# Optimization experiments

Measured on AMD Instinct MI355X. Metric: run time of the kernel, lower is better.

Reference implementation:

```python
import jax, jax.numpy as jnp
import numpy as np

B, N, T, D = 4, 256, 64, 128
DR, DH = 32, 128  # d_relation, d_hidden


def setup_inputs() -> dict:
    key = jax.random.key(0)
    ks = jax.random.split(key, 12)
    s = 0.05
    return {
        "H": jax.random.normal(ks[0], (B, N, T, D), jnp.float32),
        "R": jax.random.normal(ks[1], (B, N, N, DR), jnp.float32),
        "delta_H": jax.random.normal(ks[2], (B, N, T, D), jnp.float32),
        # params (torch Linear convention: W @ x + b with W shape (out, in))
        "Wq": jax.random.normal(ks[3], (DH, D), jnp.float32) * s,
        "bq": jnp.zeros((DH,), jnp.float32),
        "Wk": jax.random.normal(ks[4], (DH, D), jnp.float32) * s,
        "bk": jnp.zeros((DH,), jnp.float32),
        "Wr": jax.random.normal(ks[5], (DH, DR), jnp.float32) * s,
        "br": jnp.zeros((DH,), jnp.float32),
        "Wf": jax.random.normal(ks[6], (D, 3 * D + DR), jnp.float32) * s,
        "bf": jnp.zeros((D,), jnp.float32),
        "gamma": jnp.ones((D,), jnp.float32),
        "beta": jnp.zeros((D,), jnp.float32),
    }


def reference(H, R, delta_H, Wq, bq, Wk, bk, Wr, br, Wf, bf, gamma, beta):
    Bm, Nn, Tt, Dd = H.shape
    dr = R.shape[-1]

    # projections (eval mode: dropout is identity)
    q = jnp.einsum('bitd,hd->bith', H, Wq) + bq           # (B,N,T,DH)
    k = jnp.einsum('bjtd,hd->bjth', H, Wk) + bk           # (B,N,T,DH)
    rproj = jnp.einsum('bijr,hr->bijh', R, Wr) + br       # (B,N,N,DH)

    # attn_score[b,i,j,t] = <q_i[t], k_j[t] + Wr(r_ij)> / sqrt(d_model)
    scores = (jnp.einsum('bith,bjth->bijt', q, k)
              + jnp.einsum('bith,bijh->bijt', q, rproj)) / jnp.sqrt(jnp.asarray(Dd, H.dtype))
    w = jax.nn.softmax(scores, axis=-1)                   # softmax over time t
    # exclude the j == i pair (original loop skips it)
    w = w * (1.0 - jnp.eye(Nn, dtype=w.dtype))[None, :, :, None]

    # fuse Linear decomposed over the concat [h_i, h_j, r_ij, sum_t delta_h_j]
    W1 = Wf[:, :Dd]                 # acts on h_i
    W2 = Wf[:, Dd:2 * Dd]           # acts on h_j
    W3 = Wf[:, 2 * Dd:2 * Dd + dr]  # acts on r_ij
    W4 = Wf[:, 2 * Dd + dr:]        # acts on delta sum

    A = jnp.einsum('bitd,ed->bite', H, W1)                       # (B,N,T,D)
    Bj = jnp.einsum('bjtd,ed->bjte', H, W2)                      # (B,N,T,D)
    Cij = jnp.einsum('bijr,er->bije', R, W3)                     # (B,N,N,D)
    Ej = jnp.einsum('bjd,ed->bje', delta_H.sum(axis=2), W4)      # (B,N,D)

    wsum = w.sum(axis=2)                                         # (B,N,T)
    z = ((A + bf) * wsum[..., None]
         + jnp.einsum('bijt,bjte->bite', w, Bj)
         + jnp.einsum('bijt,bije->bite', w, Cij)
         + jnp.einsum('bijt,bje->bite', w, Ej))

    # residual + LayerNorm over last dim
    x = H + z
    mu = x.mean(axis=-1, keepdims=True)
    var = x.var(axis=-1, keepdims=True)
    return (x - mu) / jnp.sqrt(var + 1e-5) * gamma + beta
```

## Files before the change

### kernel.cpp

```cpp
#include <hip/hip_runtime.h>

typedef __attribute__((ext_vector_type(4))) float f32x4;
typedef __attribute__((ext_vector_type(8))) short short8;

constexpr int NB = 4, NS = 256, NT = 64, ND = 128, NR = 32;
constexpr int WFR = 3 * ND + NR;
constexpr float SCALE = 0.08838834764831845f;

__device__ __forceinline__ unsigned short f2bf(float f) {
  unsigned x = __float_as_uint(f);
  return (unsigned short)((x + 0x7FFFu + ((x >> 16) & 1u)) >> 16);
}
__device__ __forceinline__ float bf2f(unsigned short u) {
  return __uint_as_float((unsigned)u << 16);
}

__global__ __launch_bounds__(256) void kP(const float* __restrict__ Wq,
    const float* __restrict__ Wk, const float* __restrict__ Wr,
    const float* __restrict__ br, const float* __restrict__ bq,
    const float* __restrict__ Wf,
    unsigned short* __restrict__ Wqb, unsigned short* __restrict__ Wkb,
    unsigned short* __restrict__ W1b, unsigned short* __restrict__ W2b,
    unsigned short* __restrict__ W3b, unsigned short* __restrict__ Wqrt,
    float* __restrict__ Gbias) {
  const int blk = blockIdx.x, tid = threadIdx.x;
  if (blk < 64) {
    const int which = blk >> 4;
    const int idx = ((blk & 15) * 256 + tid) * 4;
    const int e = idx >> 7, d = idx & 127;
    float4 v;
    unsigned short* dst;
    if (which == 0)      { v = *(const float4*)&Wq[idx];            dst = Wqb; }
    else if (which == 1) { v = *(const float4*)&Wk[idx];            dst = Wkb; }
    else if (which == 2) { v = *(const float4*)&Wf[e * WFR + d];        dst = W1b; }
    else                 { v = *(const float4*)&Wf[e * WFR + ND + d];   dst = W2b; }
    dst[idx + 0] = f2bf(v.x); dst[idx + 1] = f2bf(v.y);
    dst[idx + 2] = f2bf(v.z); dst[idx + 3] = f2bf(v.w);
  } else if (blk < 68) {
    const int idx = ((blk - 64) * 256 + tid) * 4;
    const int e = idx >> 5, r = idx & 31;
    float4 v = *(const float4*)&Wf[e * WFR + 2 * ND + r];
    W3b[idx + 0] = f2bf(v.x); W3b[idx + 1] = f2bf(v.y);
    W3b[idx + 2] = f2bf(v.z); W3b[idx + 3] = f2bf(v.w);
  } else {
    const int rr = blk - 68;
    __shared__ float Vl[128];
    __shared__ float gbl[128];
    if (tid < 128) {
      float v = 0.f;
      if (rr < 32) v = Wr[tid * 32 + rr];
      else if (rr == 32) v = br[tid];
      Vl[tid] = v;
      gbl[tid] = bq[tid] * v;
    }
    __syncthreads();
    if (tid < 128) {
      float acc = 0.f;
      #pragma unroll 8
      for (int h = 0; h < 128; ++h) acc += Wq[h * 128 + tid] * Vl[h];
      Wqrt[rr * 128 + tid] = f2bf(acc * SCALE);
    }
    if (tid == 0) {
      float g = 0.f;
      for (int h = 0; h < 128; ++h) g += gbl[h];
      Gbias[rr] = g * SCALE;
    }
  }
}

__global__ __launch_bounds__(128) void kA(const float* __restrict__ dH,
                                          const float* __restrict__ Wf,
                                          float* __restrict__ Ej) {
  __shared__ float ds[ND];
  const int bj = blockIdx.x;
  const int d = threadIdx.x;
  const float* p = dH + (size_t)bj * NT * ND + d;
  float s = 0.f;
  #pragma unroll 8
  for (int t = 0; t < NT; ++t) s += p[t * ND];
  ds[d] = s;
  __syncthreads();
  const float* w4 = Wf + (size_t)d * WFR + 2 * ND + NR;
  float acc = 0.f;
  #pragma unroll 8
  for (int dd = 0; dd < ND; ++dd) acc += ds[dd] * w4[dd];
  Ej[(size_t)bj * ND + d] = acc;
}

__global__ __launch_bounds__(256) void kR(const float* __restrict__ R,
                                          unsigned short* __restrict__ Rb,
                                          unsigned short* __restrict__ Rtb) {
  __shared__ unsigned short rt[256 * 34];
  const int bi = blockIdx.x, tid = threadIdx.x;
  const float* src = R + (size_t)bi * 8192;
  #pragma unroll
  for (int it = 0; it < 8; ++it) {
    const int idx = (tid + it * 256) * 4;
    const float4 v = *(const float4*)&src[idx];
    const unsigned short s0 = f2bf(v.x), s1 = f2bf(v.y);
    const unsigned short s2 = f2bf(v.z), s3 = f2bf(v.w);
    unsigned long long p = (unsigned long long)s0 | ((unsigned long long)s1 << 16)
                         | ((unsigned long long)s2 << 32) | ((unsigned long long)s3 << 48);
    *(unsigned long long*)&Rb[(size_t)bi * 8192 + idx] = p;
    const int j = idx >> 5, r = idx & 31;
    *(unsigned*)&rt[j * 34 + r]     = (unsigned)s0 | ((unsigned)s1 << 16);
    *(unsigned*)&rt[j * 34 + r + 2] = (unsigned)s2 | ((unsigned)s3 << 16);
  }
  __syncthreads();
  #pragma unroll
  for (int it = 0; it < 4; ++it) {
    const int flat = (tid + it * 256) * 8;
    const int r = flat >> 8, j0 = flat & 255;
    short8 o;
    #pragma unroll
    for (int u = 0; u < 8; ++u) o[u] = (short)rt[(j0 + u) * 34 + r];
    *(short8*)&Rtb[(size_t)bi * 8192 + flat] = o;
  }
}

__device__ __forceinline__ void gemm_tile(const short8 (&afr)[4][4],
    const unsigned short* __restrict__ Wp, int nt, int l15, int l4,
    f32x4 (&acc)[4]) {
  #pragma unroll
  for (int mt = 0; mt < 4; ++mt) acc[mt] = (f32x4){0.f, 0.f, 0.f, 0.f};
  #pragma unroll
  for (int kt = 0; kt < 4; ++kt) {
    short8 bfr = *(const short8*)(Wp + (16 * nt + l15) * 128 + 32 * kt + 8 * l4);
    #pragma unroll
    for (int mt = 0; mt < 4; ++mt)
      acc[mt] = __builtin_amdgcn_mfma_f32_16x16x32_bf16(afr[mt][kt], bfr, acc[mt], 0, 0, 0);
  }
}

__global__ __launch_bounds__(256) void kB(const float* __restrict__ H,
    const unsigned short* __restrict__ Wqb, const unsigned short* __restrict__ Wkb,
    const unsigned short* __restrict__ W1b, const unsigned short* __restrict__ W2b,
    const unsigned short* __restrict__ Wqrt, const float* __restrict__ Gbias,
    const float* __restrict__ bq, const float* __restrict__ bk,
    const float* __restrict__ bf, const float* __restrict__ Ej,
    unsigned short* __restrict__ qb, unsigned short* __restrict__ kb,
    unsigned short* __restrict__ Apbb, unsigned short* __restrict__ BEb,
    unsigned short* __restrict__ Gb) {
  __shared__ unsigned short st[4][64 * 136];
  const int bn = blockIdx.x, tid = threadIdx.x;
  const int b = bn >> 8, n = bn & 255;
  const int lane = tid & 63, wv = tid >> 6;
  const int l15 = lane & 15, l4 = lane >> 4;
  short8 afr[4][4];
  const float* hb = H + (size_t)bn * (NT * ND);
  #pragma unroll
  for (int mt = 0; mt < 4; ++mt)
    #pragma unroll
    for (int kt = 0; kt < 4; ++kt) {
      const float* p = hb + (16 * mt + l15) * ND + 32 * kt + 8 * l4;
      float4 u0 = *(const float4*)p;
      float4 u1 = *(const float4*)(p + 4);
      short8 f;
      f[0] = (short)f2bf(u0.x); f[1] = (short)f2bf(u0.y);
      f[2] = (short)f2bf(u0.z); f[3] = (short)f2bf(u0.w);
      f[4] = (short)f2bf(u1.x); f[5] = (short)f2bf(u1.y);
      f[6] = (short)f2bf(u1.z); f[7] = (short)f2bf(u1.w);
      afr[mt][kt] = f;
    }
  f32x4 acc[4];
  #pragma unroll 1
  for (int pass = 0; pass < 4; ++pass) {
    const unsigned short* W = (pass == 0) ? Wqb : (pass == 1) ? Wkb
                            : (pass == 2) ? W1b : W2b;
    unsigned short* buf = st[pass];
    #pragma unroll
    for (int n2 = 0; n2 < 2; ++n2) {
      const int nt = 2 * wv + n2, c = 16 * nt + l15;
      gemm_tile(afr, W, nt, l15, l4, acc);
      const float bias = (pass == 0) ? bq[c] : (pass == 1) ? bk[c]
                       : (pass == 2) ? bf[c] : Ej[(size_t)bn * 128 + c];
      #pragma unroll
      for (int mt = 0; mt < 4; ++mt)
        #pragma unroll
        for (int jr = 0; jr < 4; ++jr)
          buf[(16 * mt + 4 * l4 + jr) * 136 + c] = f2bf(acc[mt][jr] + bias);
    }
  }
  if (wv < 3) {
    const int nt = wv, c = 16 * nt + l15;
    gemm_tile(afr, Wqrt, nt, l15, l4, acc);
    const float bias = Gbias[c];
    #pragma unroll
    for (int mt = 0; mt < 4; ++mt)
      #pragma unroll
      for (int jr = 0; jr < 4; ++jr) {
        const int tr = 16 * mt + 4 * l4 + jr;
        Gb[(size_t)bn * 3072 + tr * 48 + c] = f2bf(acc[mt][jr] + bias);
      }
  }
  __syncthreads();
  const int row0 = tid >> 4, col = 8 * (tid & 15);
  #pragma unroll
  for (int it = 0; it < 4; ++it) {
    const int row = row0 + it * 16;
    *(short8*)&qb[((size_t)(b * 64 + row) * 256 + n) * 128 + col] =
        *(const short8*)&st[0][row * 136 + col];
    *(short8*)&kb[((size_t)(b * 64 + row) * 256 + n) * 128 + col] =
        *(const short8*)&st[1][row * 136 + col];
    *(short8*)&Apbb[(size_t)bn * 8192 + row * 128 + col] =
        *(const short8*)&st[2][row * 136 + col];
    *(short8*)&BEb[((size_t)(b * 64 + row) * 256 + n) * 128 + col] =
        *(const short8*)&st[3][row * 136 + col];
  }
}

__global__ __launch_bounds__(512) void kC1(const unsigned short* __restrict__ qb,
    const unsigned short* __restrict__ kb, unsigned short* __restrict__ Sb) {
  __shared__ unsigned short st[8][32 * 136];
  const int bt = blockIdx.x, jq = blockIdx.y;
  const int tid = threadIdx.x, lane = tid & 63, wv = tid >> 6;
  const int l15 = lane & 15, l4 = lane >> 4;
  const unsigned short* qslice = qb + (size_t)bt * (256 * 128);
  const unsigned short* kslice = kb + (size_t)bt * (256 * 128);
  f32x4 acc[2][8];
  #pragma unroll
  for (int mi = 0; mi < 2; ++mi)
    #pragma unroll
    for (int nt = 0; nt < 8; ++nt) acc[mi][nt] = (f32x4){0.f, 0.f, 0.f, 0.f};
  #pragma unroll
  for (int kt = 0; kt < 4; ++kt) {
    short8 a[2], bb[8];
    #pragma unroll
    for (int mi = 0; mi < 2; ++mi) {
      const int i = 32 * wv + 16 * mi + l15;
      a[mi] = *(const short8*)(qslice + i * 128 + 32 * kt + 8 * l4);
    }
    #pragma unroll
    for (int nt = 0; nt < 8; ++nt) {
      const int j = 128 * jq + 16 * nt + l15;
      bb[nt] = *(const short8*)(kslice + j * 128 + 32 * kt + 8 * l4);
    }
    #pragma unroll
    for (int mi = 0; mi < 2; ++mi)
      #pragma unroll
      for (int nt = 0; nt < 8; ++nt)
        acc[mi][nt] = __builtin_amdgcn_mfma_f32_16x16x32_bf16(a[mi], bb[nt], acc[mi][nt], 0, 0, 0);
  }
  unsigned short* buf = st[wv];
  #pragma unroll
  for (int mi = 0; mi < 2; ++mi)
    #pragma unroll
    for (int nt = 0; nt < 8; ++nt)
      #pragma unroll
      for (int jr = 0; jr < 4; ++jr)
        buf[(16 * mi + 4 * l4 + jr) * 136 + 16 * nt + l15] =
            f2bf(acc[mi][nt][jr] * SCALE);
  #pragma unroll
  for (int it = 0; it < 8; ++it) {
    const int flat = lane * 8 + it * 512;
    const int row = flat >> 7, col = flat & 127;
    const int i = 32 * wv + row;
    *(short8*)&Sb[((size_t)bt * 256 + i) * 256 + 128 * jq + col] =
        *(const short8*)&buf[row * 136 + col];
  }
}

__global__ __launch_bounds__(256) void kSM(
    const unsigned short* __restrict__ Gb, const unsigned short* __restrict__ Rb,
    const unsigned short* __restrict__ Rtb, const unsigned short* __restrict__ Sb,
    const unsigned short* __restrict__ W3b, unsigned short* __restrict__ Apbb,
    unsigned short* __restrict__ Wbw) {
  __shared__ unsigned short wl[64 * 264];
  __shared__ unsigned short Ml[4][16 * 40];
  __shared__ float wred[4][64];
  __shared__ float wsl[64];
  const int bi = blockIdx.x, b = bi >> 8, i = bi & 255;
  const int tid = threadIdx.x, lane = tid & 63, wv = tid >> 6;
  const int l15 = lane & 15, l4 = lane >> 4;
  const f32x4 zz = (f32x4){0.f, 0.f, 0.f, 0.f};

  #pragma unroll
  for (int it = 0; it < 8; ++it) {
    const int flat = tid * 8 + it * 2048;
    const int t = flat >> 8, col = flat & 255;
    *(short8*)&wl[t * 264 + col] =
        *(const short8*)&Sb[(((size_t)b * 64 + t) * 256 + i) * 256 + col];
  }

  short8 ga[4];
  #pragma unroll
  for (int mt = 0; mt < 4; ++mt)
    ga[mt] = *(const short8*)(Gb + ((size_t)bi * 64 + 16 * mt + l15) * 48 + 8 * l4);
  f32x4 acc[4][4];
  #pragma unroll
  for (int nt = 0; nt < 4; ++nt) {
    const int j = 64 * wv + 16 * nt + l15;
    short8 rb = *(const short8*)(Rb + ((size_t)bi * 256 + j) * 32 + 8 * l4);
    #pragma unroll
    for (int mt = 0; mt < 4; ++mt)
      acc[mt][nt] = __builtin_amdgcn_mfma_f32_16x16x32_bf16(ga[mt], rb, zz, 0, 0, 0);
  }
  float qbr[4][4];
  #pragma unroll
  for (int mt = 0; mt < 4; ++mt)
    #pragma unroll
    for (int jr = 0; jr < 4; ++jr)
      qbr[mt][jr] = bf2f(Gb[((size_t)bi * 64 + 16 * mt + 4 * l4 + jr) * 48 + 32]);

  __syncthreads();

  #pragma unroll
  for (int mt = 0; mt < 4; ++mt)
    #pragma unroll
    for (int nt = 0; nt < 4; ++nt)
      #pragma unroll
      for (int jr = 0; jr < 4; ++jr)
        acc[mt][nt][jr] += bf2f(wl[(16 * mt + 4 * l4 + jr) * 264 + 64 * wv + 16 * nt + l15])
                         + qbr[mt][jr];

  #pragma unroll
  for (int nt = 0; nt < 4; ++nt) {
    float mx = -1e30f;
    #pragma unroll
    for (int mt = 0; mt < 4; ++mt)
      #pragma unroll
      for (int jr = 0; jr < 4; ++jr) mx = fmaxf(mx, acc[mt][nt][jr]);
    mx = fmaxf(mx, __shfl_xor(mx, 16));
    mx = fmaxf(mx, __shfl_xor(mx, 32));
    float sm = 0.f;
    #pragma unroll
    for (int mt = 0; mt < 4; ++mt)
      #pragma unroll
      for (int jr = 0; jr < 4; ++jr) {
        const float e = __expf(acc[mt][nt][jr] - mx);
        acc[mt][nt][jr] = e;
        sm += e;
      }
    sm += __shfl_xor(sm, 16);
    sm += __shfl_xor(sm, 32);
    const int j = 64 * wv + 16 * nt + l15;
    const float inv = (j == i) ? 0.f : 1.f / sm;
    #pragma unroll
    for (int mt = 0; mt < 4; ++mt)
      #pragma unroll
      for (int jr = 0; jr < 4; ++jr) acc[mt][nt][jr] *= inv;
  }

  float part[4][4];
  #pragma unroll
  for (int mt = 0; mt < 4; ++mt)
    #pragma unroll
    for (int jr = 0; jr < 4; ++jr) {
      float s = 0.f;
      #pragma unroll
      for (int nt = 0; nt < 4; ++nt) s += acc[mt][nt][jr];
      part[mt][jr] = s;
    }
  #pragma unroll
  for (int m = 1; m < 16; m <<= 1)
    #pragma unroll
    for (int mt = 0; mt < 4; ++mt)
      #pragma unroll
      for (int jr = 0; jr < 4; ++jr) part[mt][jr] += __shfl_xor(part[mt][jr], m);
  if (l15 == 0) {
    #pragma unroll
    for (int mt = 0; mt < 4; ++mt)
      #pragma unroll
      for (int jr = 0; jr < 4; ++jr) wred[wv][16 * mt + 4 * l4 + jr] = part[mt][jr];
  }

  #pragma unroll
  for (int mt = 0; mt < 4; ++mt)
    #pragma unroll
    for (int nt = 0; nt < 4; ++nt)
      #pragma unroll
      for (int jr = 0; jr < 4; ++jr)
        wl[(16 * mt + 4 * l4 + jr) * 264 + 64 * wv + 16 * nt + l15] =
            f2bf(acc[mt][nt][jr]);

  __syncthreads();

  if (tid < 64) wsl[tid] = wred[0][tid] + wred[1][tid] + wred[2][tid] + wred[3][tid];

  #pragma unroll
  for (int it = 0; it < 8; ++it) {
    const int flat = tid * 8 + it * 2048;
    const int t = flat >> 8, j = flat & 255;
    *(short8*)&Wbw[(((size_t)(b * 64 + t)) * 256 + i) * 256 + j] =
        *(const short8*)&wl[t * 264 + j];
  }

  f32x4 mac[2];
  mac[0] = zz; mac[1] = zz;
  #pragma unroll
  for (int kt = 0; kt < 8; ++kt) {
    short8 a = *(const short8*)&wl[(16 * wv + l15) * 264 + 32 * kt + 8 * l4];
    #pragma unroll
    for (int nt = 0; nt < 2; ++nt) {
      short8 bb = *(const short8*)(Rtb + ((size_t)bi * 32 + 16 * nt + l15) * 256 + 32 * kt + 8 * l4);
      mac[nt] = __builtin_amdgcn_mfma_f32_16x16x32_bf16(a, bb, mac[nt], 0, 0, 0);
    }
  }
  #pragma unroll
  for (int nt = 0; nt < 2; ++nt)
    #pragma unroll
    for (int jr = 0; jr < 4; ++jr)
      Ml[wv][(4 * l4 + jr) * 40 + 16 * nt + l15] = f2bf(mac[nt][jr]);
  asm volatile("s_waitcnt lgkmcnt(0)" ::: "memory");
  short8 a2 = *(const short8*)&Ml[wv][l15 * 40 + 8 * l4];
  f32x4 tac[8];
  #pragma unroll
  for (int nt = 0; nt < 8; ++nt) {
    short8 w3 = *(const short8*)(W3b + (16 * nt + l15) * 32 + 8 * l4);
    tac[nt] = __builtin_amdgcn_mfma_f32_16x16x32_bf16(a2, w3, zz, 0, 0, 0);
  }
  __syncthreads();

  const size_t abase = (size_t)bi * 8192;
  #pragma unroll
  for (int it = 0; it < 4; ++it) {
    const int flat = tid * 8 + it * 2048;
    const int row = flat >> 7, col = flat & 127;
    *(short8*)&wl[row * 136 + col] = *(const short8*)&Apbb[abase + flat];
  }
  __syncthreads();
  #pragma unroll
  for (int jr = 0; jr < 4; ++jr) {
    const int t = 16 * wv + 4 * l4 + jr;
    const float ws = wsl[t];
    #pragma unroll
    for (int nt = 0; nt < 8; ++nt) {
      const int e = 16 * nt + l15;
      const int off = t * 136 + e;
      wl[off] = f2bf(bf2f(wl[off]) * ws + tac[nt][jr]);
    }
  }
  __syncthreads();
  #pragma unroll
  for (int it = 0; it < 4; ++it) {
    const int flat = tid * 8 + it * 2048;
    const int row = flat >> 7, col = flat & 127;
    *(short8*)&Apbb[abase + flat] = *(const short8*)&wl[row * 136 + col];
  }
}

__global__ __launch_bounds__(512) void kD(const unsigned short* __restrict__ Wb,
    const unsigned short* __restrict__ BEb, const unsigned short* __restrict__ zacc,
    const float* __restrict__ H, const float* __restrict__ gamma,
    const float* __restrict__ beta, float* __restrict__ out) {
  __shared__ unsigned short Bl[128 * 264];
  const int bt = blockIdx.x;
  const int b = bt >> 6, t = bt & 63;
  const int tid = threadIdx.x, lane = tid & 63, wv = tid >> 6;
  const int l15 = lane & 15, l4 = lane >> 4;
  {
    const int j = tid >> 1, eh = (tid & 1) * 64;
    const unsigned short* src = BEb + (size_t)bt * (256 * 128) + j * 128 + eh;
    #pragma unroll
    for (int eg = 0; eg < 8; ++eg) {
      short8 v = *(const short8*)(src + 8 * eg);
      #pragma unroll
      for (int u = 0; u < 8; ++u)
        Bl[(eh + 8 * eg + u) * 264 + j] = (unsigned short)v[u];
    }
  }
  __syncthreads();
  f32x4 acc[2][8];
  #pragma unroll
  for (int m2 = 0; m2 < 2; ++m2)
    #pragma unroll
    for (int nt = 0; nt < 8; ++nt) acc[m2][nt] = (f32x4){0.f, 0.f, 0.f, 0.f};
  #pragma unroll
  for (int kt = 0; kt < 8; ++kt) {
    short8 a[2];
    #pragma unroll
    for (int m2 = 0; m2 < 2; ++m2) {
      const int i = 32 * wv + 16 * m2 + l15;
      a[m2] = *(const short8*)(Wb + ((size_t)(b * 64 + t) * 256 + i) * 256 + 32 * kt + 8 * l4);
    }
    #pragma unroll
    for (int nt = 0; nt < 8; ++nt) {
      short8 bb = *(const short8*)(&Bl[(16 * nt + l15) * 264 + 32 * kt + 8 * l4]);
      #pragma unroll
      for (int m2 = 0; m2 < 2; ++m2)
        acc[m2][nt] = __builtin_amdgcn_mfma_f32_16x16x32_bf16(a[m2], bb, acc[m2][nt], 0, 0, 0);
    }
  }
  float gam[8], bet[8];
  #pragma unroll
  for (int nt = 0; nt < 8; ++nt) {
    const int e = 16 * nt + l15;
    gam[nt] = gamma[e];
    bet[nt] = beta[e];
  }
  #pragma unroll
  for (int m2 = 0; m2 < 2; ++m2)
    #pragma unroll
    for (int jr = 0; jr < 4; ++jr) {
      const int i = 32 * wv + 16 * m2 + 4 * l4 + jr;
      const size_t base = ((size_t)(b * 256 + i) * 64 + t) * 128;
      float x[8];
      float sm = 0.f, sq = 0.f;
      #pragma unroll
      for (int nt = 0; nt < 8; ++nt) {
        const int e = 16 * nt + l15;
        const float v = acc[m2][nt][jr] + bf2f(zacc[base + e]) + H[base + e];
        x[nt] = v;
        sm += v;
        sq += v * v;
      }
      #pragma unroll
      for (int m = 1; m < 16; m <<= 1) {
        sm += __shfl_xor(sm, m);
        sq += __shfl_xor(sq, m);
      }
      const float mu = sm * (1.f / 128.f);
      const float inv = rsqrtf(sq * (1.f / 128.f) - mu * mu + 1e-5f);
      #pragma unroll
      for (int nt = 0; nt < 8; ++nt)
        out[base + 16 * nt + l15] = (x[nt] - mu) * inv * gam[nt] + bet[nt];
    }
}

extern "C" void kernel_launch(void* const* d_in, const int* in_sizes, int n_in,
                              void* d_out, int out_size, void* d_ws, size_t ws_size,
                              hipStream_t stream) {
  (void)in_sizes; (void)n_in; (void)out_size; (void)ws_size;
  const float* H     = (const float*)d_in[0];
  const float* R     = (const float*)d_in[1];
  const float* dH    = (const float*)d_in[2];
  const float* Wq    = (const float*)d_in[3];
  const float* bq    = (const float*)d_in[4];
  const float* Wk    = (const float*)d_in[5];
  const float* bk    = (const float*)d_in[6];
  const float* Wr    = (const float*)d_in[7];
  const float* br    = (const float*)d_in[8];
  const float* Wf    = (const float*)d_in[9];
  const float* bf    = (const float*)d_in[10];
  const float* gamma = (const float*)d_in[11];
  const float* beta  = (const float*)d_in[12];
  float* out = (float*)d_out;
  char* w = (char*)d_ws;

  unsigned short* qb   = (unsigned short*)(w + 0);
  unsigned short* kb   = (unsigned short*)(w + 16777216);
  unsigned short* Wbw  = (unsigned short*)(w + 0);
  unsigned short* Sb   = (unsigned short*)(w + 33554432);
  unsigned short* Apbb = (unsigned short*)(w + 67108864);
  unsigned short* BEb  = (unsigned short*)(w + 83886080);
  unsigned short* Gb   = (unsigned short*)(w + 100663296);
  unsigned short* Rb   = (unsigned short*)(w + 106954752);
  unsigned short* Rtb  = (unsigned short*)(w + 123731968);
  float*          Ejb  = (float*)(w + 140509184);
  unsigned short* Wqb  = (unsigned short*)(w + 141033472);
  unsigned short* Wkb  = (unsigned short*)(w + 141066240);
  unsigned short* W1b  = (unsigned short*)(w + 141099008);
  unsigned short* W2b  = (unsigned short*)(w + 141131776);
  unsigned short* W3b  = (unsigned short*)(w + 141164544);
  unsigned short* Wqrt = (unsigned short*)(w + 141172736);
  float*          Gbs  = (float*)(w + 141185024);

  kP<<<dim3(116), dim3(256), 0, stream>>>(Wq, Wk, Wr, br, bq, Wf,
                                          Wqb, Wkb, W1b, W2b, W3b, Wqrt, Gbs);
  kA<<<dim3(NB * NS), dim3(128), 0, stream>>>(dH, Wf, Ejb);
  kR<<<dim3(NB * NS), dim3(256), 0, stream>>>(R, Rb, Rtb);
  kB<<<dim3(NB * NS), dim3(256), 0, stream>>>(H, Wqb, Wkb, W1b, W2b, Wqrt, Gbs,
                                              bq, bk, bf, Ejb, qb, kb, Apbb, BEb, Gb);
  kC1<<<dim3(NB * NT, 2), dim3(512), 0, stream>>>(qb, kb, Sb);
  kSM<<<dim3(NB * NS), dim3(256), 0, stream>>>(Gb, Rb, Rtb, Sb, W3b, Apbb, Wbw);
  kD<<<dim3(NB * NT), dim3(512), 0, stream>>>(Wbw, BEb, Apbb, H, gamma, beta, out);
}
```

Before: 166.0 us.

## Fuse Q/K projections into score kernel, keeping q and k in LDS

Moves the Q and K projections out of kB into a new per-(b,t) kernel that projects H for all 256 nodes into shared memory and immediately computes the QK^T score tile. This removes the bf16 q/k round trip through global memory (write in kB, read in kC1). In exchange, H is read twice (in kB and in kQK) with strided per-t access, the new kernel uses about 136KB of LDS per 512-thread block, and only 256 blocks launch. Apbb store indexing is also changed to a flat contiguous pattern.

```diff
diff --git a/kernel.cpp b/kernel.cpp
--- a/kernel.cpp
+++ b/kernel.cpp
@@ -132,16 +132,27 @@
   }
 }
 
+__device__ __forceinline__ void gemm_tile2(const short8 (&afr)[2][4],
+    const unsigned short* __restrict__ Wp, int nt, int l15, int l4,
+    f32x4 (&acc)[2]) {
+  #pragma unroll
+  for (int mt = 0; mt < 2; ++mt) acc[mt] = (f32x4){0.f, 0.f, 0.f, 0.f};
+  #pragma unroll
+  for (int kt = 0; kt < 4; ++kt) {
+    short8 bfr = *(const short8*)(Wp + (16 * nt + l15) * 128 + 32 * kt + 8 * l4);
+    #pragma unroll
+    for (int mt = 0; mt < 2; ++mt)
+      acc[mt] = __builtin_amdgcn_mfma_f32_16x16x32_bf16(afr[mt][kt], bfr, acc[mt], 0, 0, 0);
+  }
+}
+
 __global__ __launch_bounds__(256) void kB(const float* __restrict__ H,
-    const unsigned short* __restrict__ Wqb, const unsigned short* __restrict__ Wkb,
     const unsigned short* __restrict__ W1b, const unsigned short* __restrict__ W2b,
     const unsigned short* __restrict__ Wqrt, const float* __restrict__ Gbias,
-    const float* __restrict__ bq, const float* __restrict__ bk,
     const float* __restrict__ bf, const float* __restrict__ Ej,
-    unsigned short* __restrict__ qb, unsigned short* __restrict__ kb,
     unsigned short* __restrict__ Apbb, unsigned short* __restrict__ BEb,
     unsigned short* __restrict__ Gb) {
-  __shared__ unsigned short st[4][64 * 136];
+  __shared__ unsigned short st[2][64 * 136];
   const int bn = blockIdx.x, tid = threadIdx.x;
   const int b = bn >> 8, n = bn & 255;
   const int lane = tid & 63, wv = tid >> 6;
@@ -164,16 +175,14 @@
     }
   f32x4 acc[4];
   #pragma unroll 1
-  for (int pass = 0; pass < 4; ++pass) {
-    const unsigned short* W = (pass == 0) ? Wqb : (pass == 1) ? Wkb
-                            : (pass == 2) ? W1b : W2b;
+  for (int pass = 0; pass < 2; ++pass) {
+    const unsigned short* W = (pass == 0) ? W1b : W2b;
     unsigned short* buf = st[pass];
     #pragma unroll
     for (int n2 = 0; n2 < 2; ++n2) {
       const int nt = 2 * wv + n2, c = 16 * nt + l15;
       gemm_tile(afr, W, nt, l15, l4, acc);
-      const float bias = (pass == 0) ? bq[c] : (pass == 1) ? bk[c]
-                       : (pass == 2) ? bf[c] : Ej[(size_t)bn * 128 + c];
+      const float bias = (pass == 0) ? bf[c] : Ej[(size_t)bn * 128 + c];
       #pragma unroll
       for (int mt = 0; mt < 4; ++mt)
         #pragma unroll
@@ -194,69 +203,102 @@
       }
   }
   __syncthreads();
-  const int row0 = tid >> 4, col = 8 * (tid & 15);
   #pragma unroll
   for (int it = 0; it < 4; ++it) {
-    const int row = row0 + it * 16;
-    *(short8*)&qb[((size_t)(b * 64 + row) * 256 + n) * 128 + col] =
-        *(const short8*)&st[0][row * 136 + col];
-    *(short8*)&kb[((size_t)(b * 64 + row) * 256 + n) * 128 + col] =
+    const int flat = tid * 8 + it * 2048;
+    const int row = flat >> 7, col = flat & 127;
+    *(short8*)&Apbb[(size_t)bn * 8192 + flat] = *(const short8*)&st[0][row * 136 + col];
+    *(short8*)&BEb[((size_t)(b * 64 + row) * 256 + n) * 128 + col] =
         *(const short8*)&st[1][row * 136 + col];
-    *(short8*)&Apbb[(size_t)bn * 8192 + row * 128 + col] =
-        *(const short8*)&st[2][row * 136 + col];
-    *(short8*)&BEb[((size_t)(b * 64 + row) * 256 + n) * 128 + col] =
-        *(const short8*)&st[3][row * 136 + col];
-  }
-}
-
-__global__ __launch_bounds__(512) void kC1(const unsigned short* __restrict__ qb,
-    const unsigned short* __restrict__ kb, unsigned short* __restrict__ Sb) {
-  __shared__ unsigned short st[8][32 * 136];
-  const int bt = blockIdx.x, jq = blockIdx.y;
+  }
+}
+
+__global__ __launch_bounds__(512) void kQK(const float* __restrict__ H,
+    const unsigned short* __restrict__ Wqb, const unsigned short* __restrict__ Wkb,
+    const float* __restrict__ bq, const float* __restrict__ bk,
+    unsigned short* __restrict__ Sb) {
+  __shared__ unsigned short qs[256 * 136];
+  __shared__ unsigned short ks[256 * 136];
+  const int bt = blockIdx.x;
+  const int b = bt >> 6, t = bt & 63;
   const int tid = threadIdx.x, lane = tid & 63, wv = tid >> 6;
   const int l15 = lane & 15, l4 = lane >> 4;
-  const unsigned short* qslice = qb + (size_t)bt * (256 * 128);
-  const unsigned short* kslice = kb + (size_t)bt * (256 * 128);
-  f32x4 acc[2][8];
-  #pragma unroll
-  for (int mi = 0; mi < 2; ++mi)
-    #pragma unroll
-    for (int nt = 0; nt < 8; ++nt) acc[mi][nt] = (f32x4){0.f, 0.f, 0.f, 0.f};
-  #pragma unroll
-  for (int kt = 0; kt < 4; ++kt) {
-    short8 a[2], bb[8];
-    #pragma unroll
-    for (int mi = 0; mi < 2; ++mi) {
-      const int i = 32 * wv + 16 * mi + l15;
-      a[mi] = *(const short8*)(qslice + i * 128 + 32 * kt + 8 * l4);
-    }
+  short8 afr[2][4];
+  #pragma unroll
+  for (int mt = 0; mt < 2; ++mt)
+    #pragma unroll
+    for (int kt = 0; kt < 4; ++kt) {
+      const int n = 32 * wv + 16 * mt + l15;
+      const float* p = &H[(((size_t)(b * 256 + n)) * 64 + t) * 128 + 32 * kt + 8 * l4];
+      float4 u0 = *(const float4*)p;
+      float4 u1 = *(const float4*)(p + 4);
+      short8 f;
+      f[0] = (short)f2bf(u0.x); f[1] = (short)f2bf(u0.y);
+      f[2] = (short)f2bf(u0.z); f[3] = (short)f2bf(u0.w);
+      f[4] = (short)f2bf(u1.x); f[5] = (short)f2bf(u1.y);
+      f[6] = (short)f2bf(u1.z); f[7] = (short)f2bf(u1.w);
+      afr[mt][kt] = f;
+    }
+  f32x4 acc[2];
+  #pragma unroll 1
+  for (int pass = 0; pass < 2; ++pass) {
+    const unsigned short* W = (pass == 0) ? Wqb : Wkb;
+    const float* bp = (pass == 0) ? bq : bk;
+    unsigned short* dst = (pass == 0) ? qs : ks;
     #pragma unroll
     for (int nt = 0; nt < 8; ++nt) {
-      const int j = 128 * jq + 16 * nt + l15;
-      bb[nt] = *(const short8*)(kslice + j * 128 + 32 * kt + 8 * l4);
-    }
+      gemm_tile2(afr, W, nt, l15, l4, acc);
+      const int c = 16 * nt + l15;
+      const float bias = bp[c];
+      #pragma unroll
+      for (int mt = 0; mt < 2; ++mt)
+        #pragma unroll
+        for (int jr = 0; jr < 4; ++jr)
+          dst[(32 * wv + 16 * mt + 4 * l4 + jr) * 136 + c] = f2bf(acc[mt][jr] + bias);
+    }
+  }
+  __syncthreads();
+  short8 qa[2][4];
+  #pragma unroll
+  for (int mt = 0; mt < 2; ++mt)
+    #pragma unroll
+    for (int kt = 0; kt < 4; ++kt)
+      qa[mt][kt] = *(const short8*)&qs[(32 * wv + 16 * mt + l15) * 136 + 32 * kt + 8 * l4];
+  unsigned short* buf = qs + wv * (32 * 136);
+  #pragma unroll 1
+  for (int jh = 0; jh < 2; ++jh) {
+    f32x4 sacc[2][8];
     #pragma unroll
     for (int mi = 0; mi < 2; ++mi)
       #pragma unroll
-      for (int nt = 0; nt < 8; ++nt)
-        acc[mi][nt] = __builtin_amdgcn_mfma_f32_16x16x32_bf16(a[mi], bb[nt], acc[mi][nt], 0, 0, 0);
-  }
-  unsigned short* buf = st[wv];
-  #pragma unroll
-  for (int mi = 0; mi < 2; ++mi)
-    #pragma unroll
-    for (int nt = 0; nt < 8; ++nt)
-      #pragma unroll
-      for (int jr = 0; jr < 4; ++jr)
-        buf[(16 * mi + 4 * l4 + jr) * 136 + 16 * nt + l15] =
-            f2bf(acc[mi][nt][jr] * SCALE);
-  #pragma unroll
-  for (int it = 0; it < 8; ++it) {
-    const int flat = lane * 8 + it * 512;
-    const int row = flat >> 7, col = flat & 127;
-    const int i = 32 * wv + row;
-    *(short8*)&Sb[((size_t)bt * 256 + i) * 256 + 128 * jq + col] =
-        *(const short8*)&buf[row * 136 + col];
+      for (int ntj = 0; ntj < 8; ++ntj) sacc[mi][ntj] = (f32x4){0.f, 0.f, 0.f, 0.f};
+    #pragma unroll
+    for (int kt = 0; kt < 4; ++kt) {
+      short8 bb[8];
+      #pragma unroll
+      for (int ntj = 0; ntj < 8; ++ntj)
+        bb[ntj] = *(const short8*)&ks[(16 * (8 * jh + ntj) + l15) * 136 + 32 * kt + 8 * l4];
+      #pragma unroll
+      for (int mi = 0; mi < 2; ++mi)
+        #pragma unroll
+        for (int ntj = 0; ntj < 8; ++ntj)
+          sacc[mi][ntj] = __builtin_amdgcn_mfma_f32_16x16x32_bf16(qa[mi][kt], bb[ntj], sacc[mi][ntj], 0, 0, 0);
+    }
+    #pragma unroll
+    for (int mi = 0; mi < 2; ++mi)
+      #pragma unroll
+      for (int ntj = 0; ntj < 8; ++ntj)
+        #pragma unroll
+        for (int jr = 0; jr < 4; ++jr)
+          buf[(16 * mi + 4 * l4 + jr) * 136 + 16 * ntj + l15] =
+              f2bf(sacc[mi][ntj][jr] * SCALE);
+    #pragma unroll
+    for (int it = 0; it < 8; ++it) {
+      const int flat = lane * 8 + it * 512;
+      const int row = flat >> 7, col = flat & 127;
+      *(short8*)&Sb[((size_t)bt * 256 + 32 * wv + row) * 256 + 128 * jh + col] =
+          *(const short8*)&buf[row * 136 + col];
+    }
   }
 }
 
@@ -537,8 +579,6 @@
   float* out = (float*)d_out;
   char* w = (char*)d_ws;
 
-  unsigned short* qb   = (unsigned short*)(w + 0);
-  unsigned short* kb   = (unsigned short*)(w + 16777216);
   unsigned short* Wbw  = (unsigned short*)(w + 0);
   unsigned short* Sb   = (unsigned short*)(w + 33554432);
   unsigned short* Apbb = (unsigned short*)(w + 67108864);
@@ -559,9 +599,9 @@
                                           Wqb, Wkb, W1b, W2b, W3b, Wqrt, Gbs);
   kA<<<dim3(NB * NS), dim3(128), 0, stream>>>(dH, Wf, Ejb);
   kR<<<dim3(NB * NS), dim3(256), 0, stream>>>(R, Rb, Rtb);
-  kB<<<dim3(NB * NS), dim3(256), 0, stream>>>(H, Wqb, Wkb, W1b, W2b, Wqrt, Gbs,
-                                              bq, bk, bf, Ejb, qb, kb, Apbb, BEb, Gb);
-  kC1<<<dim3(NB * NT, 2), dim3(512), 0, stream>>>(qb, kb, Sb);
+  kB<<<dim3(NB * NS), dim3(256), 0, stream>>>(H, W1b, W2b, Wqrt, Gbs,
+                                              bf, Ejb, Apbb, BEb, Gb);
+  kQK<<<dim3(NB * NT), dim3(512), 0, stream>>>(H, Wqb, Wkb, bq, bk, Sb);
   kSM<<<dim3(NB * NS), dim3(256), 0, stream>>>(Gb, Rb, Rtb, Sb, W3b, Apbb, Wbw);
   kD<<<dim3(NB * NT), dim3(512), 0, stream>>>(Wbw, BEb, Apbb, H, gamma, beta, out);
 }
```

Measured after the change: 164.3 us. About the same (-1.0%).
